# Performance work log

Hardware: AMD Instinct MI355X
Metric: run time of the kernel (lower is better)

## Reference

```python
import jax, jax.numpy as jnp
import numpy as np

# ---- exact Hungarian (Jonker-Volgenant / e-maxx shortest augmenting path) ----

def _lsa(cost):
    """Square cost matrix [n,n] (numpy) -> col index assigned to each row (optimal)."""
    n = cost.shape[0]
    a = np.zeros((n + 1, n + 1), dtype=np.float64)
    a[1:, 1:] = cost
    u = np.zeros(n + 1)
    v = np.zeros(n + 1)
    p = np.zeros(n + 1, dtype=np.int64)   # p[j] = row matched to column j (1-indexed)
    way = np.zeros(n + 1, dtype=np.int64)
    for i in range(1, n + 1):
        p[0] = i
        j0 = 0
        minv = np.full(n + 1, np.inf)
        used = np.zeros(n + 1, dtype=bool)
        while True:
            used[j0] = True
            i0 = p[j0]
            cur = a[i0] - u[i0] - v
            better = (~used) & (cur < minv)
            minv[better] = cur[better]
            way[better] = j0
            masked = np.where(used, np.inf, minv)
            j1 = int(np.argmin(masked))
            delta = masked[j1]
            u[p[used]] += delta
            v[used] -= delta
            minv[~used] -= delta
            j0 = j1
            if p[j0] == 0:
                break
        while j0 != 0:
            j1 = way[j0]
            p[j0] = p[j1]
            j0 = j1
    col = np.zeros(n, dtype=np.int64)
    for j in range(1, n + 1):
        col[p[j] - 1] = j - 1
    return col


def _lsa_batch(costs):
    """costs [..., N, N] numpy -> assigned col per row [..., N]."""
    N = costs.shape[-1]
    flat = costs.reshape(-1, N, N)
    cols = np.stack([_lsa(c) for c in flat])
    return cols.reshape(costs.shape[:-1])


# ---- kernel pieces (same math as cdist_torch / material_distances) ----

def _pair_sqdist(v1, v2):
    g = jnp.einsum('pnd,bmd->pbnm', v1, v2)
    s1 = (v1 ** 2).sum(-1)
    s2 = (v2 ** 2).sum(-1)
    return jnp.abs(-2.0 * g + s1[:, None, :, None] + s2[None, :, None, :])


def _self_sqdist(v):
    # v [B,N,d] -> [B,N,N]; only diagonal pairs of Material_kernel(x,x) are needed
    g = jnp.einsum('bnd,bmd->bnm', v, v)
    s = (v ** 2).sum(-1)
    return jnp.abs(-2.0 * g + s[:, :, None] + s[:, None, :])


def _material_kernel(D2, cols):
    # sum_i exp(-D2[..., i, cols[..., i]]) / N  (Hungarian-matched similarity)
    sel = jnp.take_along_axis(D2, cols[..., None], axis=-1)[..., 0]
    return jnp.exp(-sel).sum(-1) / D2.shape[-1]


def setup_inputs():
    key = jax.random.key(0)
    ks = jax.random.split(key, 4)
    P, B, A, d = 64, 32, 40, 128
    x = jax.random.normal(ks[0], (B, A, d), jnp.float32)
    data_points = jax.random.normal(ks[1], (P, A, d), jnp.float32)
    gamma = jnp.full((1, d), -2.0, jnp.float32)  # matches __init__: ones(1,n_in)*-2
    M = jax.random.normal(ks[2], (P, P), jnp.float32)
    K = M @ M.T + P * jnp.eye(P, dtype=jnp.float32)
    L = jnp.linalg.cholesky(K).astype(jnp.float32)  # valid trained-state Cholesky buffer
    alpha = jax.random.normal(ks[3], (P,), jnp.float32)
    return {"x": x, "data_points": data_points, "gamma": gamma, "L": L, "alpha": alpha}


def reference(x, data_points, gamma, L, alpha):
    g = jnp.exp(gamma)                      # [1,d]
    v1 = data_points * g                    # [P,A,d]
    v2 = x * g                              # [B,A,d]
    D2 = _pair_sqdist(v1, v2)               # [P,B,A,A]
    cols = jnp.asarray(_lsa_batch(np.asarray(D2, np.float64)))
    K_xnew = _material_kernel(D2, cols)     # [P,B]
    Linv = jnp.linalg.inv(L)
    v = Linv @ K_xnew                       # [P,B]
    mean = jnp.einsum('in,i->n', K_xnew, alpha)
    Ds = _self_sqdist(v2)                   # [B,A,A] (diagonal of K(x,x) only)
    cols_s = jnp.asarray(_lsa_batch(np.asarray(Ds, np.float64)))
    kxx = _material_kernel(Ds, cols_s)      # [B]
    var = kxx - jnp.einsum('in,in->n', v, v)
    return mean, var
```

## Files before the change

### kernel.cpp

```cpp
#include <hip/hip_runtime.h>
#include <math.h>

#define P_N 64
#define B_N 32
#define A_N 40
#define D_N 128

__device__ __forceinline__ int readlane_i(int v, int l) {
  return __builtin_amdgcn_readlane(v, l);
}
__device__ __forceinline__ float readlane_f(float v, int l) {
  return __int_as_float(__builtin_amdgcn_readlane(__float_as_int(v), l));
}
__device__ __forceinline__ unsigned ordf(float f) {
  unsigned b = __float_as_uint(f);
  return b ^ (((unsigned)((int)b >> 31)) | 0x80000000u);
}
__device__ __forceinline__ float unordf(unsigned k) {
  unsigned b = k ^ (((unsigned)((int)(~k) >> 31)) | 0x80000000u);
  return __uint_as_float(b);
}
__device__ __forceinline__ unsigned wave_min_u32(unsigned x) {
  unsigned t;
  t = (unsigned)__builtin_amdgcn_update_dpp((int)0xFFFFFFFFu, (int)x, 0x111, 0xF, 0xF, false);
  x = t < x ? t : x;
  t = (unsigned)__builtin_amdgcn_update_dpp((int)0xFFFFFFFFu, (int)x, 0x112, 0xF, 0xF, false);
  x = t < x ? t : x;
  t = (unsigned)__builtin_amdgcn_update_dpp((int)0xFFFFFFFFu, (int)x, 0x114, 0xF, 0xF, false);
  x = t < x ? t : x;
  t = (unsigned)__builtin_amdgcn_update_dpp((int)0xFFFFFFFFu, (int)x, 0x118, 0xF, 0xF, false);
  x = t < x ? t : x;
  t = (unsigned)__builtin_amdgcn_update_dpp((int)0xFFFFFFFFu, (int)x, 0x142, 0xA, 0xF, false);
  x = t < x ? t : x;
  t = (unsigned)__builtin_amdgcn_update_dpp((int)0xFFFFFFFFu, (int)x, 0x143, 0xC, 0xF, false);
  x = t < x ? t : x;
  return (unsigned)__builtin_amdgcn_readlane((int)x, 63);
}
__device__ __forceinline__ void wave_min2_u32(unsigned x, unsigned &m1o, unsigned &m2o) {
  unsigned m1 = x, m2 = 0xFFFFFFFFu;
  unsigned t1, t2, lo, hi;
#define MIN2_STAGE(ctrl, rm) \
  t1 = (unsigned)__builtin_amdgcn_update_dpp((int)0xFFFFFFFFu, (int)m1, ctrl, rm, 0xF, false); \
  t2 = (unsigned)__builtin_amdgcn_update_dpp((int)0xFFFFFFFFu, (int)m2, ctrl, rm, 0xF, false); \
  lo = m1 < t1 ? m1 : t1; hi = m1 < t1 ? t1 : m1;                                              \
  m2 = m2 < t2 ? m2 : t2; m2 = m2 < hi ? m2 : hi; m1 = lo;
  MIN2_STAGE(0x111, 0xF)
  MIN2_STAGE(0x112, 0xF)
  MIN2_STAGE(0x114, 0xF)
  MIN2_STAGE(0x118, 0xF)
  MIN2_STAGE(0x142, 0xA)
  MIN2_STAGE(0x143, 0xC)
#undef MIN2_STAGE
  m1o = (unsigned)__builtin_amdgcn_readlane((int)m1, 63);
  m2o = (unsigned)__builtin_amdgcn_readlane((int)m2, 63);
}

__global__ __launch_bounds__(64) void hungarian_pair(
    const float* __restrict__ DP, const float* __restrict__ X,
    const float* __restrict__ G, float* __restrict__ out) {
  __shared__ float Cs[A_N * A_N];
  __shared__ float g_lds[D_N];
  const int bid  = blockIdx.x;
  const int lane = threadIdx.x;
  const float* __restrict__ Abase = DP + (bid >> 5) * (A_N * D_N);
  const float* __restrict__ Bbase = X  + (bid & 31) * (A_N * D_N);

  g_lds[lane]      = expf(G[lane]);
  g_lds[lane + 64] = expf(G[lane + 64]);
  __syncthreads();

  if (lane < A_N) {
    const float* bp = Bbase + lane * D_N;
    for (int c = 0; c < 4; ++c) {
      float4 gg[8], bb[8];
      #pragma unroll
      for (int k = 0; k < 8; ++k) {
        gg[k] = ((const float4*)(g_lds + c * 32))[k];
        float4 br = ((const float4*)(bp + c * 32))[k];
        bb[k] = make_float4(br.x * gg[k].x, br.y * gg[k].y,
                            br.z * gg[k].z, br.w * gg[k].w);
      }
      for (int i = 0; i < A_N; ++i) {
        const float4* ap = (const float4*)(Abase + i * D_N + c * 32);
        float s = 0.f;
        #pragma unroll
        for (int k = 0; k < 8; ++k) {
          float4 a = ap[k];
          float dx = fmaf(a.x, gg[k].x, -bb[k].x); s = fmaf(dx, dx, s);
          float dy = fmaf(a.y, gg[k].y, -bb[k].y); s = fmaf(dy, dy, s);
          float dz = fmaf(a.z, gg[k].z, -bb[k].z); s = fmaf(dz, dz, s);
          float dw = fmaf(a.w, gg[k].w, -bb[k].w); s = fmaf(dw, dw, s);
        }
        if (c == 0) Cs[i * A_N + lane] = s;
        else        Cs[i * A_N + lane] += s;
      }
    }
  }
  __syncthreads();

  const int  cix     = (lane >= 1 && lane <= A_N) ? (lane - 1) : 0;
  const bool realcol = (lane >= 1 && lane <= A_N);

  float vpot = 0.f;
  int   amin = 0;
  if (realcol) {
    float mn = INFINITY; int mi = 0;
    for (int i = 0; i < A_N; ++i) {
      float c = Cs[i * A_N + cix];
      if (c < mn) { mn = c; mi = i; }
    }
    vpot = mn; amin = mi + 1;
  }

  unsigned long long rmask = 0ull;
  int p = 0, way = 0;
  for (int j = 1; j <= A_N; ++j) {
    int am = readlane_i(amin, j);
    if (!((rmask >> am) & 1ull)) {
      rmask |= 1ull << am;
      if (lane == j) p = am;
    }
  }

  float u = 0.f;

  unsigned long long fmask = (((1ull << (A_N + 1)) - 2ull)) & ~rmask;
  unsigned long long dmask = 0ull;
  {
    int I = 0; bool chaining = false; int iters = 0;
    while ((chaining || fmask) && iters < 64) {
      if (!chaining) { I = __builtin_ctzll(fmask); fmask &= fmask - 1ull; }
      ++iters;
      float r = realcol ? (Cs[(I - 1) * A_N + cix] - vpot) : INFINITY;
      unsigned key = (ordf(r) & 0xFFFFFFC0u) | (unsigned)lane;
      unsigned m1, m2;
      wave_min2_u32(key, m1, m2);
      int   j1  = (int)(m1 & 63u);
      float u1  = readlane_f(r, j1);
      float u2a = unordf(m2 & 0xFFFFFFC0u);
      int   k   = readlane_i(p, j1);
      bool  strict = (u1 < u2a);
      if (strict || k == 0) {
        if (strict) {
          if (lane == j1) vpot -= (u2a - u1);
          if (lane == I)  u = u2a;
        } else {
          if (lane == I)  u = u1;
        }
        if (lane == j1) p = I;
        if (k != 0) { I = k; chaining = true; }
        else        chaining = false;
      } else {
        dmask |= 1ull << I;
        chaining = false;
      }
    }
    if (chaining) dmask |= 1ull << I;
    dmask |= fmask;
  }

  while (dmask) {
    int f = __builtin_ctzll(dmask); dmask &= dmask - 1ull;
    if (lane == 0) p = f;
    float mhat = INFINITY;
    float excl = realcol ? 0.f : INFINITY;
    float dsum = 0.f;
    float dent = 0.f, rent = 0.f;
    bool  used   = !realcol;
    bool  intree = (lane == f);
    int   j0 = 0, i0 = f;
    const unsigned plane_key = ((unsigned)p << 6) | (unsigned)lane;
    for (int guard = 0; guard < 42; ++guard) {
      float Craw = Cs[(i0 - 1) * A_N + cix];
      float uc   = readlane_f(u, i0);
      float off  = dsum - uc - vpot + excl;
      float cand = Craw + off;
      if (cand < mhat) way = j0;
      mhat = fminf(mhat, cand);
      unsigned key = (ordf(mhat) & 0xFFFFF000u) | plane_key;
      unsigned kmin = wave_min_u32(key);
      int j1 = (int)(kmin & 63u);
      int i1 = (int)((kmin >> 6) & 63u);
      float dnew = unordf(kmin & 0xFFFFF000u);
      if (lane == j1) { used = true; dent = dnew; excl = INFINITY; mhat = INFINITY; }
      dsum = dnew;
      j0 = j1;
      i0 = i1;
      if (i1 == 0) break;
      if (lane == i1) { intree = true; rent = dnew; }
    }
    if (used && realcol) vpot -= (dsum - dent);
    if (intree)          u    += (dsum - rent);
    while (j0 != 0) {
      int jn = readlane_i(way, j0);
      int pn = readlane_i(p, jn);
      if (lane == j0) p = pn;
      j0 = jn;
    }
  }

  float e = 0.f;
  if (realcol) e = expf(-Cs[(p - 1) * A_N + (lane - 1)]);
  #pragma unroll
  for (int off = 32; off; off >>= 1) e += __shfl_xor(e, off);
  if (lane == 0) out[bid] = e / 40.0f;
}

__global__ __launch_bounds__(64) void final_kernel(
    const float* __restrict__ Kx, const float* __restrict__ L,
    const float* __restrict__ alpha, float* __restrict__ out) {
  int b = threadIdx.x;
  if (b >= B_N) return;
  float mean = 0.f;
  #pragma unroll
  for (int p = 0; p < P_N; ++p) mean = fmaf(Kx[p * B_N + b], alpha[p], mean);
  out[b] = mean;
  float vr[P_N];
  float sumv2 = 0.f;
  #pragma unroll
  for (int i = 0; i < P_N; ++i) {
    float s = Kx[i * B_N + b];
    #pragma unroll
    for (int j = 0; j < i; ++j) s = fmaf(-L[i * P_N + j], vr[j], s);
    float vi = s / L[i * P_N + i];
    vr[i] = vi;
    sumv2 = fmaf(vi, vi, sumv2);
  }
  out[B_N + b] = 1.0f - sumv2;
}

extern "C" void kernel_launch(void* const* d_in, const int* in_sizes, int n_in,
                              void* d_out, int out_size, void* d_ws, size_t ws_size,
                              hipStream_t stream) {
  const float* x     = (const float*)d_in[0];
  const float* dp    = (const float*)d_in[1];
  const float* gamma = (const float*)d_in[2];
  const float* L     = (const float*)d_in[3];
  const float* alpha = (const float*)d_in[4];
  float* out = (float*)d_out;

  float* Kx = (float*)d_ws;

  hungarian_pair<<<P_N * B_N, 64, 0, stream>>>(dp, x, gamma, Kx);
  final_kernel<<<1, 64, 0, stream>>>(Kx, L, alpha, out);
}
```

Baseline: 127.7 us.

## Fuse distance computation with column-min init and use inline DPP min reduction

The cost-matrix build now keeps the whole scaled B row in registers (32 float4) and computes all 128 dims per entry in one pass. It fuses the column-minimum search for the initial dual potentials into that pass, removing the separate LDS re-read and the four read-modify-write passes over Cs. The wave min reduction is rewritten as inline asm v_min_u32 with DPP modifiers so each stage is a single instruction instead of update_dpp plus compare. launch_bounds adds a min-blocks hint of 2, which with the larger register footprint may cap registers and cause spills.

```diff
diff --git a/kernel.cpp b/kernel.cpp
--- a/kernel.cpp
+++ b/kernel.cpp
@@ -21,19 +21,12 @@
   return __uint_as_float(b);
 }
 __device__ __forceinline__ unsigned wave_min_u32(unsigned x) {
-  unsigned t;
-  t = (unsigned)__builtin_amdgcn_update_dpp((int)0xFFFFFFFFu, (int)x, 0x111, 0xF, 0xF, false);
-  x = t < x ? t : x;
-  t = (unsigned)__builtin_amdgcn_update_dpp((int)0xFFFFFFFFu, (int)x, 0x112, 0xF, 0xF, false);
-  x = t < x ? t : x;
-  t = (unsigned)__builtin_amdgcn_update_dpp((int)0xFFFFFFFFu, (int)x, 0x114, 0xF, 0xF, false);
-  x = t < x ? t : x;
-  t = (unsigned)__builtin_amdgcn_update_dpp((int)0xFFFFFFFFu, (int)x, 0x118, 0xF, 0xF, false);
-  x = t < x ? t : x;
-  t = (unsigned)__builtin_amdgcn_update_dpp((int)0xFFFFFFFFu, (int)x, 0x142, 0xA, 0xF, false);
-  x = t < x ? t : x;
-  t = (unsigned)__builtin_amdgcn_update_dpp((int)0xFFFFFFFFu, (int)x, 0x143, 0xC, 0xF, false);
-  x = t < x ? t : x;
+  asm volatile("s_nop 1\n\tv_min_u32 %0, %0, %0 row_shr:1"  : "+v"(x));
+  asm volatile("s_nop 1\n\tv_min_u32 %0, %0, %0 row_shr:2"  : "+v"(x));
+  asm volatile("s_nop 1\n\tv_min_u32 %0, %0, %0 row_shr:4"  : "+v"(x));
+  asm volatile("s_nop 1\n\tv_min_u32 %0, %0, %0 row_shr:8"  : "+v"(x));
+  asm volatile("s_nop 1\n\tv_min_u32 %0, %0, %0 row_bcast:15 row_mask:0xa" : "+v"(x));
+  asm volatile("s_nop 1\n\tv_min_u32 %0, %0, %0 row_bcast:31 row_mask:0xc" : "+v"(x));
   return (unsigned)__builtin_amdgcn_readlane((int)x, 63);
 }
 __device__ __forceinline__ void wave_min2_u32(unsigned x, unsigned &m1o, unsigned &m2o) {
@@ -55,7 +48,7 @@
   m2o = (unsigned)__builtin_amdgcn_readlane((int)m2, 63);
 }
 
-__global__ __launch_bounds__(64) void hungarian_pair(
+__global__ __launch_bounds__(64, 2) void hungarian_pair(
     const float* __restrict__ DP, const float* __restrict__ X,
     const float* __restrict__ G, float* __restrict__ out) {
   __shared__ float Cs[A_N * A_N];
@@ -69,48 +62,39 @@
   g_lds[lane + 64] = expf(G[lane + 64]);
   __syncthreads();
 
-  if (lane < A_N) {
-    const float* bp = Bbase + lane * D_N;
-    for (int c = 0; c < 4; ++c) {
-      float4 gg[8], bb[8];
-      #pragma unroll
-      for (int k = 0; k < 8; ++k) {
-        gg[k] = ((const float4*)(g_lds + c * 32))[k];
-        float4 br = ((const float4*)(bp + c * 32))[k];
-        bb[k] = make_float4(br.x * gg[k].x, br.y * gg[k].y,
-                            br.z * gg[k].z, br.w * gg[k].w);
-      }
-      for (int i = 0; i < A_N; ++i) {
-        const float4* ap = (const float4*)(Abase + i * D_N + c * 32);
-        float s = 0.f;
-        #pragma unroll
-        for (int k = 0; k < 8; ++k) {
-          float4 a = ap[k];
-          float dx = fmaf(a.x, gg[k].x, -bb[k].x); s = fmaf(dx, dx, s);
-          float dy = fmaf(a.y, gg[k].y, -bb[k].y); s = fmaf(dy, dy, s);
-          float dz = fmaf(a.z, gg[k].z, -bb[k].z); s = fmaf(dz, dz, s);
-          float dw = fmaf(a.w, gg[k].w, -bb[k].w); s = fmaf(dw, dw, s);
-        }
-        if (c == 0) Cs[i * A_N + lane] = s;
-        else        Cs[i * A_N + lane] += s;
-      }
-    }
-  }
-  __syncthreads();
-
   const int  cix     = (lane >= 1 && lane <= A_N) ? (lane - 1) : 0;
   const bool realcol = (lane >= 1 && lane <= A_N);
 
   float vpot = 0.f;
   int   amin = 0;
   if (realcol) {
+    const float* bp = Bbase + cix * D_N;
+    float4 bb[32];
+    #pragma unroll
+    for (int k = 0; k < 32; ++k) {
+      float4 gr = ((const float4*)g_lds)[k];
+      float4 br = ((const float4*)bp)[k];
+      bb[k] = make_float4(br.x * gr.x, br.y * gr.y, br.z * gr.z, br.w * gr.w);
+    }
     float mn = INFINITY; int mi = 0;
-    for (int i = 0; i < A_N; ++i) {
-      float c = Cs[i * A_N + cix];
-      if (c < mn) { mn = c; mi = i; }
+    for (int r = 0; r < A_N; ++r) {
+      const float4* __restrict__ ap = (const float4*)(Abase + r * D_N);
+      float s = 0.f;
+      #pragma unroll
+      for (int k = 0; k < 32; ++k) {
+        float4 a  = ap[k];
+        float4 gr = ((const float4*)g_lds)[k];
+        float dx = fmaf(a.x, gr.x, -bb[k].x); s = fmaf(dx, dx, s);
+        float dy = fmaf(a.y, gr.y, -bb[k].y); s = fmaf(dy, dy, s);
+        float dz = fmaf(a.z, gr.z, -bb[k].z); s = fmaf(dz, dz, s);
+        float dw = fmaf(a.w, gr.w, -bb[k].w); s = fmaf(dw, dw, s);
+      }
+      Cs[r * A_N + cix] = s;
+      if (s < mn) { mn = s; mi = r; }
     }
     vpot = mn; amin = mi + 1;
   }
+  __syncthreads();
 
   unsigned long long rmask = 0ull;
   int p = 0, way = 0;
```

Measured after the change: 147.0 us. 1.15x slower.
